# Optimization experiments

Measured on AMD Instinct MI355X. Metric: run time of the kernel, lower is better.

The kernel has to match this reference:

```python
import jax, jax.numpy as jnp
import numpy as np

N_FFT = 254
WIN = 254
HOP = 64
ITERS = 50
AUDIO_DIM = 16384
MAX_VALUE = 69.37411499023438


def _hann(n):
    # tf.signal.hann_window (periodic)
    return (0.5 - 0.5 * jnp.cos(2.0 * jnp.pi * jnp.arange(n) / n)).astype(jnp.float32)


def _synth_window():
    # tf.signal.inverse_stft_window_fn(HOP) applied to hann forward window
    w = _hann(WIN)
    overlaps = -(-WIN // HOP)
    d = jnp.pad(w * w, (0, overlaps * HOP - WIN))
    d = d.reshape(overlaps, HOP).sum(axis=0)  # overlap-added squared window per phase
    d = jnp.tile(d, overlaps)[:WIN]
    return w / d


def _stft(x, window):
    # x: [B, L] -> [B, F, N_FFT//2+1]; win_length == n_fft so no zero-padding of frames
    L = x.shape[1]
    nf = 1 + (L - WIN) // HOP
    idx = jnp.arange(nf)[:, None] * HOP + jnp.arange(WIN)
    frames = x[:, idx] * window
    return jnp.fft.rfft(frames, n=N_FFT)


def _istft(spec, swin, out_len):
    # spec: [B, F, bins] -> [B, out_len] via windowed overlap-add
    frames = jnp.fft.irfft(spec, n=N_FFT)[..., :WIN] * swin
    nf = frames.shape[1]
    idx = jnp.arange(nf)[:, None] * HOP + jnp.arange(WIN)
    out = jnp.zeros((frames.shape[0], out_len), frames.dtype)
    return out.at[:, idx].add(frames)


def setup_inputs() -> dict:
    key = jax.random.key(0)
    x = jax.random.uniform(key, (128, 256, 128, 1), dtype=jnp.float32)
    return {"x": x}


def reference(x):
    win = _hann(WIN)
    swin = _synth_window()
    # de-log / de-normalize the spectrogram
    mag = jnp.exp(5.0 * (x - 1.0)) * MAX_VALUE
    mag = jnp.squeeze(mag, -1)  # [B, F, 128]
    nframes = mag.shape[1]
    out_len = HOP * (nframes - 1) + WIN  # 16574

    # Griffin-Lim: initial reconstruction with zero phase
    waveform = _istft(mag.astype(jnp.complex64), swin, out_len)

    def step(wf, _):
        phase = jnp.angle(_stft(wf, win))
        spec = mag * jnp.exp(1j * phase)
        return _istft(spec, swin, out_len), None

    waveform, _ = jax.lax.scan(step, waveform, None, length=ITERS)

    waveform = waveform / jnp.max(jnp.abs(waveform))
    return waveform[:, :AUDIO_DIM, None]  # [B, 16384, 1]
```

## Files before the change

### kernel.cpp

```cpp
#include <hip/hip_runtime.h>
#include <math.h>


#define B_SZ 128
#define NFRM 256
#define BINS 128
#define NFFT 254
#define OUTL 16574
#define AUD  16384
#define GL_ITERS 50
#define MAXV 69.37411499023438f
#define PI2f 6.2831853071795864f

typedef __attribute__((ext_vector_type(8))) short short8;
typedef __attribute__((ext_vector_type(4))) short short4v;
typedef __attribute__((ext_vector_type(4))) float f32x4;

__device__ __forceinline__ unsigned short f2bf(float f) {
  unsigned u = __float_as_uint(f);
  return (unsigned short)((u + 0x7FFFu + ((u >> 16) & 1u)) >> 16);
}
__device__ __forceinline__ float bf2f(unsigned short h) {
  return __uint_as_float(((unsigned)h) << 16);
}
__device__ __forceinline__ void split3(float v, short* h, short* m, short* l) {
  unsigned short hh = f2bf(v);
  float r1 = v - bf2f(hh);
  unsigned short mm = f2bf(r1);
  float r2 = r1 - bf2f(mm);
  *h = (short)hh; *m = (short)mm; *l = (short)f2bf(r2);
}

__device__ __forceinline__ int slotf(int c, int row) {
  return (c & ~7) | ((c ^ row ^ (row >> 3)) & 7);
}

#define MFMA6(ACC, AH, AM, AL, BH, BM, BL)                                   \
  ACC = __builtin_amdgcn_mfma_f32_16x16x32_bf16(AH, BL, ACC, 0, 0, 0);       \
  ACC = __builtin_amdgcn_mfma_f32_16x16x32_bf16(AM, BM, ACC, 0, 0, 0);       \
  ACC = __builtin_amdgcn_mfma_f32_16x16x32_bf16(AL, BH, ACC, 0, 0, 0);       \
  ACC = __builtin_amdgcn_mfma_f32_16x16x32_bf16(AH, BM, ACC, 0, 0, 0);       \
  ACC = __builtin_amdgcn_mfma_f32_16x16x32_bf16(AM, BH, ACC, 0, 0, 0);       \
  ACC = __builtin_amdgcn_mfma_f32_16x16x32_bf16(AH, BH, ACC, 0, 0, 0);

__global__ void tables_k(short* __restrict__ WfH, short* __restrict__ WfM,
                         short* __restrict__ WfL, short* __restrict__ WiH,
                         short* __restrict__ WiM, short* __restrict__ WiL,
                         unsigned* __restrict__ gmax) {
  int tid = blockIdx.x * blockDim.x + threadIdx.x;
  if (tid == 0) *gmax = 0u;
  if (tid >= 65536) return;
  int idx = tid;
  int j = idx & 7, l = (idx >> 3) & 63, nt = (idx >> 9) & 15, kc = idx >> 13;
  int krow = kc * 32 + ((l >> 4) << 3) + j;
  int ncol = (nt << 4) + (l & 15);
  float v1 = 0.f;
  if (krow < NFFT) {
    int kk = ncol >> 1;
    int m = (kk * krow) % NFFT;
    float ang = PI2f * (float)m / (float)NFFT;
    float wn = 0.5f - 0.5f * cosf(PI2f * (float)krow / (float)NFFT);
    v1 = wn * ((ncol & 1) ? -sinf(ang) : cosf(ang));
  }
  split3(v1, &WfH[idx], &WfM[idx], &WfL[idx]);
  float v2 = 0.f;
  if (ncol < NFFT) {
    int kk = krow >> 1;
    int m = (kk * ncol) % NFFT;
    float ang = PI2f * (float)m / (float)NFFT;
    float wn = 0.5f - 0.5f * cosf(PI2f * (float)ncol / (float)NFFT);
    float d = 0.f;
    int p = ncol & 63;
    for (int q = 0; q < 4; ++q) {
      int nn = p + 64 * q;
      if (nn < NFFT) { float w = 0.5f - 0.5f * cosf(PI2f * (float)nn / (float)NFFT); d += w * w; }
    }
    float sw = wn / d;
    float ak = (kk == 0 || kk == BINS - 1) ? 1.f : 2.f;
    v2 = sw * (ak / (float)NFFT) * ((krow & 1) ? -sinf(ang) : cosf(ang));
  }
  split3(v2, &WiH[idx], &WiM[idx], &WiL[idx]);
}

__global__ void mag_k(const float* __restrict__ x, float* __restrict__ mag) {
  int i = blockIdx.x * 256 + threadIdx.x;
  mag[i] = expf(5.f * (x[i] - 1.f)) * MAXV;
}

template <int FIRST>
__global__ __launch_bounds__(512) void iter_k(
    const float* __restrict__ FRsrc, float* __restrict__ FRdst,
    const float* __restrict__ mag,
    const short* __restrict__ WfH, const short* __restrict__ WfM,
    const short* __restrict__ WfL,
    const short* __restrict__ WiH, const short* __restrict__ WiM,
    const short* __restrict__ WiL) {
  __shared__ __align__(16) short SH[8192], SM[8192], SL[8192];
  __shared__ __align__(16) char scratch[16640];
  short* wfsH = (short*)scratch;
  short* wfsM = wfsH + 2240;
  short* wfsL = wfsM + 2240;
  float* tr = (float*)scratch;

  int blk = blockIdx.x;
  int b = blk >> 3, f0 = (blk & 7) << 5;
  int tid = threadIdx.x, lane = tid & 63, wv = tid >> 6;
  int fgl = b * NFRM + f0;

  if (FIRST) {
    int row = tid >> 4;
#pragma unroll
    for (int q = 0; q < 2; ++q) {
      int c = ((tid & 15) << 1) + q;
      float4 mg = *(const float4*)&mag[((size_t)(fgl + row) << 7) + (c << 2)];
      short h[8] __attribute__((aligned(16))), m[8] __attribute__((aligned(16))),
            l[8] __attribute__((aligned(16)));
#pragma unroll
      for (int u = 0; u < 4; ++u) {
        split3(((const float*)&mg)[u], &h[2 * u], &m[2 * u], &l[2 * u]);
        h[2 * u + 1] = 0; m[2 * u + 1] = 0; l[2 * u + 1] = 0;
      }
      int p = (row << 8) + (slotf(c, row) << 3);
      *(short8*)&SH[p] = *(const short8*)h;
      *(short8*)&SM[p] = *(const short8*)m;
      *(short8*)&SL[p] = *(const short8*)l;
    }
  } else {
    const float* FRb = FRsrc + ((size_t)b << 16);
    for (int i4 = tid; i4 < 560; i4 += 512) {
      int i = i4 << 2;
      int t = (f0 << 6) + i;
      int ft = t >> 6, cb = t & 63;
      float4 s = make_float4(0.f, 0.f, 0.f, 0.f);
#pragma unroll
      for (int d = 3; d >= 0; --d) {
        int f = ft - d;
        if (f >= 0 && f <= 255) {
          float4 v = *(const float4*)&FRb[(f << 8) + cb + (d << 6)];
          s.x += v.x; s.y += v.y; s.z += v.z; s.w += v.w;
        }
      }
      if (i == 2236) { s.z = 0.f; s.w = 0.f; }
      short hh[4] __attribute__((aligned(8))), mm[4] __attribute__((aligned(8))),
            ll[4] __attribute__((aligned(8)));
      split3(s.x, &hh[0], &mm[0], &ll[0]);
      split3(s.y, &hh[1], &mm[1], &ll[1]);
      split3(s.z, &hh[2], &mm[2], &ll[2]);
      split3(s.w, &hh[3], &mm[3], &ll[3]);
      int q = i >> 3;
      int qs = (q & ~7) | ((q ^ (q >> 3)) & 7);
      int p = (qs << 3) | (i & 7);
      *(short4v*)&wfsH[p] = *(const short4v*)hh;
      *(short4v*)&wfsM[p] = *(const short4v*)mm;
      *(short4v*)&wfsL[p] = *(const short4v*)ll;
    }

    f32x4 acc1[2][2];
#pragma unroll
    for (int i = 0; i < 2; ++i) { acc1[i][0] = (f32x4){0,0,0,0}; acc1[i][1] = (f32x4){0,0,0,0}; }

    __syncthreads();

    for (int kc = 0; kc < 8; ++kc) {
      short8 Ah[2], Am[2], Al[2];
#pragma unroll
      for (int mt = 0; mt < 2; ++mt) {
        int frame = (mt << 4) + (lane & 15);
        int q = (frame << 3) + (kc << 2) + (lane >> 4);
        int qs = (q & ~7) | ((q ^ (q >> 3)) & 7);
        Ah[mt] = *(const short8*)&wfsH[qs << 3];
        Am[mt] = *(const short8*)&wfsM[qs << 3];
        Al[mt] = *(const short8*)&wfsL[qs << 3];
      }
#pragma unroll
      for (int nt = 0; nt < 2; ++nt) {
        int ntg = (wv << 1) + nt;
        size_t off = (((size_t)((kc << 4) + ntg) << 6) + lane) << 3;
        short8 bh = *(const short8*)(WfH + off);
        short8 bm = *(const short8*)(WfM + off);
        short8 bl = *(const short8*)(WfL + off);
#pragma unroll
        for (int mt = 0; mt < 2; ++mt) {
          MFMA6(acc1[mt][nt], Ah[mt], Am[mt], Al[mt], bh, bm, bl)
        }
      }
    }

    for (int mtg = 0; mtg < 2; ++mtg) {
      __syncthreads();
#pragma unroll
      for (int nt = 0; nt < 2; ++nt) {
        int col = (((wv << 1) + nt) << 4) | (lane & 15);
#pragma unroll
        for (int r = 0; r < 4; ++r) {
          int row16 = ((lane >> 4) << 2) + r;
          tr[row16 * 260 + col] = acc1[mtg][nt][r];
        }
      }
      __syncthreads();
      {
        int trow = tid >> 5;
        int c = tid & 31;
        int c0 = c << 3;
        float4 va = *(const float4*)&tr[trow * 260 + c0];
        float4 vb = *(const float4*)&tr[trow * 260 + c0 + 4];
        int lrow = (mtg << 4) + trow;
        int srow = fgl + lrow;
        float4 xm = *(const float4*)&mag[((size_t)srow << 7) + (c << 2)];
        float vv[8] = {va.x, va.y, va.z, va.w, vb.x, vb.y, vb.z, vb.w};
        short hh[8] __attribute__((aligned(16))), mm[8] __attribute__((aligned(16))),
              ll[8] __attribute__((aligned(16)));
#pragma unroll
        for (int pq = 0; pq < 4; ++pq) {
          float mg = ((const float*)&xm)[pq];
          float re = vv[2 * pq], im = vv[2 * pq + 1];
          float s2 = re * re + im * im;
          float oe, oo;
          if (s2 == 0.f) { oe = mg; oo = 0.f; }
          else { float rr = mg * rsqrtf(s2); oe = re * rr; oo = im * rr; }
          split3(oe, &hh[2 * pq], &mm[2 * pq], &ll[2 * pq]);
          split3(oo, &hh[2 * pq + 1], &mm[2 * pq + 1], &ll[2 * pq + 1]);
        }
        int p = (lrow << 8) + (slotf(c, lrow) << 3);
        *(short8*)&SH[p] = *(const short8*)hh;
        *(short8*)&SM[p] = *(const short8*)mm;
        *(short8*)&SL[p] = *(const short8*)ll;
      }
    }
  }

  f32x4 acc2[2][2];
#pragma unroll
  for (int i = 0; i < 2; ++i) { acc2[i][0] = (f32x4){0,0,0,0}; acc2[i][1] = (f32x4){0,0,0,0}; }

  __syncthreads();

  for (int kc = 0; kc < 8; ++kc) {
    short8 bh[2], bm[2], bl[2];
#pragma unroll
    for (int nt = 0; nt < 2; ++nt) {
      int ntg = (wv << 1) + nt;
      size_t off = (((size_t)((kc << 4) + ntg) << 6) + lane) << 3;
      bh[nt] = *(const short8*)(WiH + off);
      bm[nt] = *(const short8*)(WiM + off);
      bl[nt] = *(const short8*)(WiL + off);
    }
#pragma unroll
    for (int mt = 0; mt < 2; ++mt) {
      int rl = (mt << 4) + (lane & 15);
      int c = (kc << 2) + (lane >> 4);
      int base = (rl << 8) + (slotf(c, rl) << 3);
      short8 Ah = *(const short8*)&SH[base];
      short8 Am = *(const short8*)&SM[base];
      short8 Al = *(const short8*)&SL[base];
#pragma unroll
      for (int nt = 0; nt < 2; ++nt) {
        MFMA6(acc2[mt][nt], Ah, Am, Al, bh[nt], bm[nt], bl[nt])
      }
    }
  }

  float* FRo = FRdst + ((size_t)b << 16) + ((size_t)f0 << 8);
#pragma unroll
  for (int mt = 0; mt < 2; ++mt)
#pragma unroll
    for (int nt = 0; nt < 2; ++nt) {
      int col = (((wv << 1) + nt) << 4) | (lane & 15);
#pragma unroll
      for (int r = 0; r < 4; ++r) {
        int row = (mt << 4) + ((lane >> 4) << 2) + r;
        FRo[((size_t)row << 8) + col] = acc2[mt][nt][r];
      }
    }
}

__global__ void redmax_k(const float* __restrict__ FR, unsigned* __restrict__ gmax) {
  __shared__ float red[16];
  int b = blockIdx.x;
  const float* FRb = FR + ((size_t)b << 16);
  float v = 0.f;
  for (int t = threadIdx.x; t < OUTL; t += 1024) {
    int f_hi = t >> 6; if (f_hi > NFRM - 1) f_hi = NFRM - 1;
    int f_lo = (t >= NFFT) ? (((t - NFFT) >> 6) + 1) : 0;
    float s = 0.f;
    for (int f = f_lo; f <= f_hi; ++f) s += FRb[(f << 8) + t - (f << 6)];
    v = fmaxf(v, fabsf(s));
  }
#pragma unroll
  for (int o = 32; o > 0; o >>= 1) v = fmaxf(v, __shfl_xor(v, o, 64));
  if ((threadIdx.x & 63) == 0) red[threadIdx.x >> 6] = v;
  __syncthreads();
  if (threadIdx.x < 16) {
    v = red[threadIdx.x];
#pragma unroll
    for (int o = 8; o > 0; o >>= 1) v = fmaxf(v, __shfl_xor(v, o, 16));
    if (threadIdx.x == 0) atomicMax(gmax, __float_as_uint(v));
  }
}

__global__ void out_k(const float* __restrict__ FR, const unsigned* __restrict__ gmax,
                      float* __restrict__ out) {
  int b = blockIdx.y, t = blockIdx.x * 256 + threadIdx.x;
  const float* FRb = FR + ((size_t)b << 16);
  int f_hi = t >> 6; if (f_hi > NFRM - 1) f_hi = NFRM - 1;
  int f_lo = (t >= NFFT) ? (((t - NFFT) >> 6) + 1) : 0;
  float s = 0.f;
  for (int f = f_lo; f <= f_hi; ++f) s += FRb[(f << 8) + t - (f << 6)];
  float g = __uint_as_float(*gmax);
  out[(size_t)b * AUD + t] = s / g;
}

extern "C" void kernel_launch(void* const* d_in, const int* in_sizes, int n_in,
                              void* d_out, int out_size, void* d_ws, size_t ws_size,
                              hipStream_t stream) {
  const float* x = (const float*)d_in[0];

  float* FR0 = (float*)d_ws;
  float* FR1 = FR0 + 8388608;
  float* mag = FR1 + 8388608;
  short* WfH = (short*)(mag + 4194304);
  short* WfM = WfH + 65536;
  short* WfL = WfM + 65536;
  short* WiH = WfL + 65536;
  short* WiM = WiH + 65536;
  short* WiL = WiM + 65536;
  unsigned* gmax = (unsigned*)(WiL + 65536);

  mag_k<<<16384, 256, 0, stream>>>(x, mag);
  tables_k<<<256, 256, 0, stream>>>(WfH, WfM, WfL, WiH, WiM, WiL, gmax);

  iter_k<1><<<1024, 512, 0, stream>>>(FR1, FR0, mag, WfH, WfM, WfL, WiH, WiM, WiL);

  float* bufs[2] = {FR0, FR1};
  for (int it = 0; it < GL_ITERS; ++it) {
    iter_k<0><<<1024, 512, 0, stream>>>(bufs[it & 1], bufs[(it + 1) & 1], mag,
                                        WfH, WfM, WfL, WiH, WiM, WiL);
  }

  redmax_k<<<B_SZ, 1024, 0, stream>>>(FR0, gmax);
  out_k<<<dim3(64, B_SZ), 256, 0, stream>>>(FR0, gmax, (float*)d_out);
}
```

Measured before the change: 2.499 ms.

## Double-buffer DFT basis loads in registers and split transpose scratch

Prefetches the next k-chunk of the forward and inverse DFT basis fragments into registers while the current chunk's MFMAs run, and preloads the first inverse chunk before the phase-projection stage. This is meant to hide global-memory latency for basis loads. It also splits the transpose scratch into two half-buffers with stride 132 to cut LDS bank conflicts. The extra live short8 registers raise register pressure, which could lower occupancy.

```diff
diff --git a/kernel.cpp b/kernel.cpp
--- a/kernel.cpp
+++ b/kernel.cpp
@@ -96,16 +96,20 @@
     const short* __restrict__ WiH, const short* __restrict__ WiM,
     const short* __restrict__ WiL) {
   __shared__ __align__(16) short SH[8192], SM[8192], SL[8192];
-  __shared__ __align__(16) char scratch[16640];
+  __shared__ __align__(16) char scratch[16896];
   short* wfsH = (short*)scratch;
   short* wfsM = wfsH + 2240;
   short* wfsL = wfsM + 2240;
-  float* tr = (float*)scratch;
+  float* trA = (float*)scratch;
+  float* trB = trA + 2112;
 
   int blk = blockIdx.x;
   int b = blk >> 3, f0 = (blk & 7) << 5;
   int tid = threadIdx.x, lane = tid & 63, wv = tid >> 6;
   int fgl = b * NFRM + f0;
+  int ntg0 = (wv << 1), ntg1 = ntg0 + 1;
+
+  short8 g2h[2][2], g2m[2][2], g2l[2][2];
 
   if (FIRST) {
     int row = tid >> 4;
@@ -125,7 +129,23 @@
       *(short8*)&SM[p] = *(const short8*)m;
       *(short8*)&SL[p] = *(const short8*)l;
     }
+    {
+      size_t o0 = (((size_t)ntg0 << 6) + lane) << 3;
+      size_t o1 = (((size_t)ntg1 << 6) + lane) << 3;
+      g2h[0][0] = *(const short8*)(WiH + o0); g2h[0][1] = *(const short8*)(WiH + o1);
+      g2m[0][0] = *(const short8*)(WiM + o0); g2m[0][1] = *(const short8*)(WiM + o1);
+      g2l[0][0] = *(const short8*)(WiL + o0); g2l[0][1] = *(const short8*)(WiL + o1);
+    }
   } else {
+    short8 g1h[2][2], g1m[2][2], g1l[2][2];
+    {
+      size_t o0 = (((size_t)ntg0 << 6) + lane) << 3;
+      size_t o1 = (((size_t)ntg1 << 6) + lane) << 3;
+      g1h[0][0] = *(const short8*)(WfH + o0); g1h[0][1] = *(const short8*)(WfH + o1);
+      g1m[0][0] = *(const short8*)(WfM + o0); g1m[0][1] = *(const short8*)(WfM + o1);
+      g1l[0][0] = *(const short8*)(WfL + o0); g1l[0][1] = *(const short8*)(WfL + o1);
+    }
+
     const float* FRb = FRsrc + ((size_t)b << 16);
     for (int i4 = tid; i4 < 560; i4 += 512) {
       int i = i4 << 2;
@@ -161,7 +181,16 @@
 
     __syncthreads();
 
+#pragma unroll
     for (int kc = 0; kc < 8; ++kc) {
+      const int cur = kc & 1, nxt = cur ^ 1;
+      if (kc < 7) {
+        size_t o0 = (((size_t)(((kc + 1) << 4) + ntg0) << 6) + lane) << 3;
+        size_t o1 = (((size_t)(((kc + 1) << 4) + ntg1) << 6) + lane) << 3;
+        g1h[nxt][0] = *(const short8*)(WfH + o0); g1h[nxt][1] = *(const short8*)(WfH + o1);
+        g1m[nxt][0] = *(const short8*)(WfM + o0); g1m[nxt][1] = *(const short8*)(WfM + o1);
+        g1l[nxt][0] = *(const short8*)(WfL + o0); g1l[nxt][1] = *(const short8*)(WfL + o1);
+      }
       short8 Ah[2], Am[2], Al[2];
 #pragma unroll
       for (int mt = 0; mt < 2; ++mt) {
@@ -173,17 +202,19 @@
         Al[mt] = *(const short8*)&wfsL[qs << 3];
       }
 #pragma unroll
-      for (int nt = 0; nt < 2; ++nt) {
-        int ntg = (wv << 1) + nt;
-        size_t off = (((size_t)((kc << 4) + ntg) << 6) + lane) << 3;
-        short8 bh = *(const short8*)(WfH + off);
-        short8 bm = *(const short8*)(WfM + off);
-        short8 bl = *(const short8*)(WfL + off);
+      for (int nt = 0; nt < 2; ++nt)
 #pragma unroll
         for (int mt = 0; mt < 2; ++mt) {
-          MFMA6(acc1[mt][nt], Ah[mt], Am[mt], Al[mt], bh, bm, bl)
+          MFMA6(acc1[mt][nt], Ah[mt], Am[mt], Al[mt], g1h[cur][nt], g1m[cur][nt], g1l[cur][nt])
         }
-      }
+    }
+
+    {
+      size_t o0 = (((size_t)ntg0 << 6) + lane) << 3;
+      size_t o1 = (((size_t)ntg1 << 6) + lane) << 3;
+      g2h[0][0] = *(const short8*)(WiH + o0); g2h[0][1] = *(const short8*)(WiH + o1);
+      g2m[0][0] = *(const short8*)(WiM + o0); g2m[0][1] = *(const short8*)(WiM + o1);
+      g2l[0][0] = *(const short8*)(WiL + o0); g2l[0][1] = *(const short8*)(WiL + o1);
     }
 
     for (int mtg = 0; mtg < 2; ++mtg) {
@@ -191,19 +222,21 @@
 #pragma unroll
       for (int nt = 0; nt < 2; ++nt) {
         int col = (((wv << 1) + nt) << 4) | (lane & 15);
+        int cc = col >> 3, hb = (col >> 2) & 1, w = col & 3;
+        float* th = hb ? trB : trA;
+        int base = (cc << 2) + w;
 #pragma unroll
         for (int r = 0; r < 4; ++r) {
           int row16 = ((lane >> 4) << 2) + r;
-          tr[row16 * 260 + col] = acc1[mtg][nt][r];
+          th[row16 * 132 + base] = acc1[mtg][nt][r];
         }
       }
       __syncthreads();
       {
         int trow = tid >> 5;
         int c = tid & 31;
-        int c0 = c << 3;
-        float4 va = *(const float4*)&tr[trow * 260 + c0];
-        float4 vb = *(const float4*)&tr[trow * 260 + c0 + 4];
+        float4 va = *(const float4*)&trA[trow * 132 + (c << 2)];
+        float4 vb = *(const float4*)&trB[trow * 132 + (c << 2)];
         int lrow = (mtg << 4) + trow;
         int srow = fgl + lrow;
         float4 xm = *(const float4*)&mag[((size_t)srow << 7) + (c << 2)];
@@ -235,15 +268,15 @@
 
   __syncthreads();
 
+#pragma unroll
   for (int kc = 0; kc < 8; ++kc) {
-    short8 bh[2], bm[2], bl[2];
-#pragma unroll
-    for (int nt = 0; nt < 2; ++nt) {
-      int ntg = (wv << 1) + nt;
-      size_t off = (((size_t)((kc << 4) + ntg) << 6) + lane) << 3;
-      bh[nt] = *(const short8*)(WiH + off);
-      bm[nt] = *(const short8*)(WiM + off);
-      bl[nt] = *(const short8*)(WiL + off);
+    const int cur = kc & 1, nxt = cur ^ 1;
+    if (kc < 7) {
+      size_t o0 = (((size_t)(((kc + 1) << 4) + ntg0) << 6) + lane) << 3;
+      size_t o1 = (((size_t)(((kc + 1) << 4) + ntg1) << 6) + lane) << 3;
+      g2h[nxt][0] = *(const short8*)(WiH + o0); g2h[nxt][1] = *(const short8*)(WiH + o1);
+      g2m[nxt][0] = *(const short8*)(WiM + o0); g2m[nxt][1] = *(const short8*)(WiM + o1);
+      g2l[nxt][0] = *(const short8*)(WiL + o0); g2l[nxt][1] = *(const short8*)(WiL + o1);
     }
 #pragma unroll
     for (int mt = 0; mt < 2; ++mt) {
@@ -255,7 +288,7 @@
       short8 Al = *(const short8*)&SL[base];
 #pragma unroll
       for (int nt = 0; nt < 2; ++nt) {
-        MFMA6(acc2[mt][nt], Ah, Am, Al, bh[nt], bm[nt], bl[nt])
+        MFMA6(acc2[mt][nt], Ah, Am, Al, g2h[cur][nt], g2m[cur][nt], g2l[cur][nt])
       }
     }
   }
```

Result: no change. 2.524 ms (+1.0%).

## Exploit real-signal symmetry in inverse DFT to halve iSTFT matmul work

Applied to the files above, without the earlier changes.

The inverse real DFT is split into a cosine part on the real spectrum and a sine part on the imaginary spectrum. Each part covers only the first half of the output samples, and the mirrored samples come from the sum and difference C±S. The synthesis window is applied in the epilogue instead of being folded into the table. This halves the MFMA count and the inverse-table loads of the second GEMM, at the cost of a new spectrum layout in LDS, an extra window table, and edge-case handling at n=0, n=127 and indices 254/255.

```diff
diff --git a/kernel.cpp b/kernel.cpp
--- a/kernel.cpp
+++ b/kernel.cpp
@@ -30,7 +30,6 @@
   float r2 = r1 - bf2f(mm);
   *h = (short)hh; *m = (short)mm; *l = (short)f2bf(r2);
 }
-
 __device__ __forceinline__ int slotf(int c, int row) {
   return (c & ~7) | ((c ^ row ^ (row >> 3)) & 7);
 }
@@ -44,42 +43,49 @@
   ACC = __builtin_amdgcn_mfma_f32_16x16x32_bf16(AH, BH, ACC, 0, 0, 0);
 
 __global__ void tables_k(short* __restrict__ WfH, short* __restrict__ WfM,
-                         short* __restrict__ WfL, short* __restrict__ WiH,
-                         short* __restrict__ WiM, short* __restrict__ WiL,
+                         short* __restrict__ WfL, short* __restrict__ CI,
+                         short* __restrict__ SI, float* __restrict__ swin,
                          unsigned* __restrict__ gmax) {
   int tid = blockIdx.x * blockDim.x + threadIdx.x;
   if (tid == 0) *gmax = 0u;
-  if (tid >= 65536) return;
-  int idx = tid;
-  int j = idx & 7, l = (idx >> 3) & 63, nt = (idx >> 9) & 15, kc = idx >> 13;
-  int krow = kc * 32 + ((l >> 4) << 3) + j;
-  int ncol = (nt << 4) + (l & 15);
-  float v1 = 0.f;
-  if (krow < NFFT) {
-    int kk = ncol >> 1;
-    int m = (kk * krow) % NFFT;
+  if (tid < 256) {
+    float v = 0.f;
+    if (tid < NFFT) {
+      float wn = 0.5f - 0.5f * cosf(PI2f * (float)tid / (float)NFFT);
+      float d = 0.f;
+      int p = tid & 63;
+      for (int q = 0; q < 4; ++q) {
+        int nn = p + 64 * q;
+        if (nn < NFFT) { float w = 0.5f - 0.5f * cosf(PI2f * (float)nn / (float)NFFT); d += w * w; }
+      }
+      v = wn / d;
+    }
+    swin[tid] = v;
+  }
+  if (tid < 65536) {
+    int j = tid & 7, l = (tid >> 3) & 63, nt = (tid >> 9) & 15, kc = tid >> 13;
+    int krow = kc * 32 + ((l >> 4) << 3) + j;
+    int ncol = (nt << 4) + (l & 15);
+    float v1 = 0.f;
+    if (krow < NFFT) {
+      int kk = ncol >> 1;
+      int m = (kk * krow) % NFFT;
+      float ang = PI2f * (float)m / (float)NFFT;
+      float wn = 0.5f - 0.5f * cosf(PI2f * (float)krow / (float)NFFT);
+      v1 = wn * ((ncol & 1) ? -sinf(ang) : cosf(ang));
+    }
+    split3(v1, &WfH[tid], &WfM[tid], &WfL[tid]);
+  }
+  if (tid < 16384) {
+    int j = tid & 7, l = (tid >> 3) & 63;
+    int krow = (tid >> 12) * 32 + ((l >> 4) << 3) + j;
+    int ncol = (((tid >> 9) & 7) << 4) + (l & 15);
+    int m = (krow * ncol) % NFFT;
     float ang = PI2f * (float)m / (float)NFFT;
-    float wn = 0.5f - 0.5f * cosf(PI2f * (float)krow / (float)NFFT);
-    v1 = wn * ((ncol & 1) ? -sinf(ang) : cosf(ang));
-  }
-  split3(v1, &WfH[idx], &WfM[idx], &WfL[idx]);
-  float v2 = 0.f;
-  if (ncol < NFFT) {
-    int kk = krow >> 1;
-    int m = (kk * ncol) % NFFT;
-    float ang = PI2f * (float)m / (float)NFFT;
-    float wn = 0.5f - 0.5f * cosf(PI2f * (float)ncol / (float)NFFT);
-    float d = 0.f;
-    int p = ncol & 63;
-    for (int q = 0; q < 4; ++q) {
-      int nn = p + 64 * q;
-      if (nn < NFFT) { float w = 0.5f - 0.5f * cosf(PI2f * (float)nn / (float)NFFT); d += w * w; }
-    }
-    float sw = wn / d;
-    float ak = (kk == 0 || kk == BINS - 1) ? 1.f : 2.f;
-    v2 = sw * (ak / (float)NFFT) * ((krow & 1) ? -sinf(ang) : cosf(ang));
-  }
-  split3(v2, &WiH[idx], &WiM[idx], &WiL[idx]);
+    float sc = ((krow == 0 || krow == BINS - 1) ? 1.f : 2.f) / (float)NFFT;
+    split3(sc * cosf(ang), &CI[tid], &CI[16384 + tid], &CI[32768 + tid]);
+    split3(-sc * sinf(ang), &SI[tid], &SI[16384 + tid], &SI[32768 + tid]);
+  }
 }
 
 __global__ void mag_k(const float* __restrict__ x, float* __restrict__ mag) {
@@ -90,17 +96,17 @@
 template <int FIRST>
 __global__ __launch_bounds__(512) void iter_k(
     const float* __restrict__ FRsrc, float* __restrict__ FRdst,
-    const float* __restrict__ mag,
+    const float* __restrict__ mag, const float* __restrict__ swin,
     const short* __restrict__ WfH, const short* __restrict__ WfM,
     const short* __restrict__ WfL,
-    const short* __restrict__ WiH, const short* __restrict__ WiM,
-    const short* __restrict__ WiL) {
-  __shared__ __align__(16) short SH[8192], SM[8192], SL[8192];
-  __shared__ __align__(16) char scratch[16640];
+    const short* __restrict__ CI, const short* __restrict__ SI) {
+  __shared__ __align__(16) short Y[24576];
+  __shared__ __align__(16) char scratch[16896];
   short* wfsH = (short*)scratch;
   short* wfsM = wfsH + 2240;
   short* wfsL = wfsM + 2240;
-  float* tr = (float*)scratch;
+  float* trA = (float*)scratch;
+  float* trB = trA + 2112;
 
   int blk = blockIdx.x;
   int b = blk >> 3, f0 = (blk & 7) << 5;
@@ -108,23 +114,22 @@
   int fgl = b * NFRM + f0;
 
   if (FIRST) {
-    int row = tid >> 4;
-#pragma unroll
-    for (int q = 0; q < 2; ++q) {
-      int c = ((tid & 15) << 1) + q;
-      float4 mg = *(const float4*)&mag[((size_t)(fgl + row) << 7) + (c << 2)];
-      short h[8] __attribute__((aligned(16))), m[8] __attribute__((aligned(16))),
-            l[8] __attribute__((aligned(16)));
-#pragma unroll
-      for (int u = 0; u < 4; ++u) {
-        split3(((const float*)&mg)[u], &h[2 * u], &m[2 * u], &l[2 * u]);
-        h[2 * u + 1] = 0; m[2 * u + 1] = 0; l[2 * u + 1] = 0;
-      }
-      int p = (row << 8) + (slotf(c, row) << 3);
-      *(short8*)&SH[p] = *(const short8*)h;
-      *(short8*)&SM[p] = *(const short8*)m;
-      *(short8*)&SL[p] = *(const short8*)l;
-    }
+    int row = tid >> 4, q = tid & 15;
+    int srow = fgl + row;
+    float4 m0 = *(const float4*)&mag[((size_t)srow << 7) + (q << 3)];
+    float4 m1 = *(const float4*)&mag[((size_t)srow << 7) + (q << 3) + 4];
+    float mv[8] = {m0.x, m0.y, m0.z, m0.w, m1.x, m1.y, m1.z, m1.w};
+    short h[8] __attribute__((aligned(16))), m[8] __attribute__((aligned(16))),
+          l[8] __attribute__((aligned(16))), z[8] __attribute__((aligned(16)));
+#pragma unroll
+    for (int e = 0; e < 8; ++e) { split3(mv[e], &h[e], &m[e], &l[e]); z[e] = 0; }
+    int off = (row << 7) + (slotf(q, row) << 3);
+    *(short8*)&Y[off]         = *(const short8*)h;
+    *(short8*)&Y[4096 + off]  = *(const short8*)m;
+    *(short8*)&Y[8192 + off]  = *(const short8*)l;
+    *(short8*)&Y[12288 + off] = *(const short8*)z;
+    *(short8*)&Y[16384 + off] = *(const short8*)z;
+    *(short8*)&Y[20480 + off] = *(const short8*)z;
   } else {
     const float* FRb = FRsrc + ((size_t)b << 16);
     for (int i4 = tid; i4 < 560; i4 += 512) {
@@ -191,87 +196,101 @@
 #pragma unroll
       for (int nt = 0; nt < 2; ++nt) {
         int col = (((wv << 1) + nt) << 4) | (lane & 15);
+        int cc = col >> 3, hb = (col >> 2) & 1, w = col & 3;
+        float* th = hb ? trB : trA;
+        int base = (cc << 2) + w;
 #pragma unroll
         for (int r = 0; r < 4; ++r) {
           int row16 = ((lane >> 4) << 2) + r;
-          tr[row16 * 260 + col] = acc1[mtg][nt][r];
+          th[row16 * 132 + base] = acc1[mtg][nt][r];
         }
       }
       __syncthreads();
       {
         int trow = tid >> 5;
         int c = tid & 31;
-        int c0 = c << 3;
-        float4 va = *(const float4*)&tr[trow * 260 + c0];
-        float4 vb = *(const float4*)&tr[trow * 260 + c0 + 4];
+        float4 va = *(const float4*)&trA[trow * 132 + (c << 2)];
+        float4 vb = *(const float4*)&trB[trow * 132 + (c << 2)];
         int lrow = (mtg << 4) + trow;
         int srow = fgl + lrow;
         float4 xm = *(const float4*)&mag[((size_t)srow << 7) + (c << 2)];
         float vv[8] = {va.x, va.y, va.z, va.w, vb.x, vb.y, vb.z, vb.w};
-        short hh[8] __attribute__((aligned(16))), mm[8] __attribute__((aligned(16))),
-              ll[8] __attribute__((aligned(16)));
+        short reh[4] __attribute__((aligned(8))), rem[4] __attribute__((aligned(8))),
+              rel[4] __attribute__((aligned(8))), imh[4] __attribute__((aligned(8))),
+              imm[4] __attribute__((aligned(8))), iml[4] __attribute__((aligned(8)));
 #pragma unroll
         for (int pq = 0; pq < 4; ++pq) {
           float mg = ((const float*)&xm)[pq];
           float re = vv[2 * pq], im = vv[2 * pq + 1];
           float s2 = re * re + im * im;
-          float oe, oo;
-          if (s2 == 0.f) { oe = mg; oo = 0.f; }
-          else { float rr = mg * rsqrtf(s2); oe = re * rr; oo = im * rr; }
-          split3(oe, &hh[2 * pq], &mm[2 * pq], &ll[2 * pq]);
-          split3(oo, &hh[2 * pq + 1], &mm[2 * pq + 1], &ll[2 * pq + 1]);
+          float ore, oim;
+          if (s2 == 0.f) { ore = mg; oim = 0.f; }
+          else { float rr = mg * rsqrtf(s2); ore = re * rr; oim = im * rr; }
+          split3(ore, &reh[pq], &rem[pq], &rel[pq]);
+          split3(oim, &imh[pq], &imm[pq], &iml[pq]);
         }
-        int p = (lrow << 8) + (slotf(c, lrow) << 3);
-        *(short8*)&SH[p] = *(const short8*)hh;
-        *(short8*)&SM[p] = *(const short8*)mm;
-        *(short8*)&SL[p] = *(const short8*)ll;
-      }
-    }
-  }
-
-  f32x4 acc2[2][2];
-#pragma unroll
-  for (int i = 0; i < 2; ++i) { acc2[i][0] = (f32x4){0,0,0,0}; acc2[i][1] = (f32x4){0,0,0,0}; }
+        int c2 = c >> 1, half = (c & 1) << 2;
+        int off2 = (lrow << 7) + (slotf(c2, lrow) << 3) + half;
+        *(short4v*)&Y[off2]         = *(const short4v*)reh;
+        *(short4v*)&Y[4096 + off2]  = *(const short4v*)rem;
+        *(short4v*)&Y[8192 + off2]  = *(const short4v*)rel;
+        *(short4v*)&Y[12288 + off2] = *(const short4v*)imh;
+        *(short4v*)&Y[16384 + off2] = *(const short4v*)imm;
+        *(short4v*)&Y[20480 + off2] = *(const short4v*)iml;
+      }
+    }
+  }
+
+  f32x4 aC[2], aS[2];
+#pragma unroll
+  for (int i = 0; i < 2; ++i) { aC[i] = (f32x4){0,0,0,0}; aS[i] = (f32x4){0,0,0,0}; }
 
   __syncthreads();
 
-  for (int kc = 0; kc < 8; ++kc) {
-    short8 bh[2], bm[2], bl[2];
-#pragma unroll
-    for (int nt = 0; nt < 2; ++nt) {
-      int ntg = (wv << 1) + nt;
-      size_t off = (((size_t)((kc << 4) + ntg) << 6) + lane) << 3;
-      bh[nt] = *(const short8*)(WiH + off);
-      bm[nt] = *(const short8*)(WiM + off);
-      bl[nt] = *(const short8*)(WiL + off);
-    }
+  for (int kc = 0; kc < 4; ++kc) {
+    short8 ReH[2], ReM[2], ReL[2], ImH[2], ImM[2], ImL[2];
 #pragma unroll
     for (int mt = 0; mt < 2; ++mt) {
       int rl = (mt << 4) + (lane & 15);
       int c = (kc << 2) + (lane >> 4);
-      int base = (rl << 8) + (slotf(c, rl) << 3);
-      short8 Ah = *(const short8*)&SH[base];
-      short8 Am = *(const short8*)&SM[base];
-      short8 Al = *(const short8*)&SL[base];
-#pragma unroll
-      for (int nt = 0; nt < 2; ++nt) {
-        MFMA6(acc2[mt][nt], Ah, Am, Al, bh[nt], bm[nt], bl[nt])
-      }
-    }
-  }
-
-  float* FRo = FRdst + ((size_t)b << 16) + ((size_t)f0 << 8);
-#pragma unroll
-  for (int mt = 0; mt < 2; ++mt)
-#pragma unroll
-    for (int nt = 0; nt < 2; ++nt) {
-      int col = (((wv << 1) + nt) << 4) | (lane & 15);
+      int off = (rl << 7) + (slotf(c, rl) << 3);
+      ReH[mt] = *(const short8*)&Y[off];
+      ReM[mt] = *(const short8*)&Y[4096 + off];
+      ReL[mt] = *(const short8*)&Y[8192 + off];
+      ImH[mt] = *(const short8*)&Y[12288 + off];
+      ImM[mt] = *(const short8*)&Y[16384 + off];
+      ImL[mt] = *(const short8*)&Y[20480 + off];
+    }
+    size_t flat = (((size_t)((kc << 3) + wv) << 6) + lane) << 3;
+    short8 ch = *(const short8*)(CI + flat);
+    short8 cm = *(const short8*)(CI + 16384 + flat);
+    short8 cl = *(const short8*)(CI + 32768 + flat);
+    short8 sh = *(const short8*)(SI + flat);
+    short8 sm = *(const short8*)(SI + 16384 + flat);
+    short8 sl = *(const short8*)(SI + 32768 + flat);
+#pragma unroll
+    for (int mt = 0; mt < 2; ++mt) {
+      MFMA6(aC[mt], ReH[mt], ReM[mt], ReL[mt], ch, cm, cl)
+      MFMA6(aS[mt], ImH[mt], ImM[mt], ImL[mt], sh, sm, sl)
+    }
+  }
+
+  {
+    int n = (wv << 4) + (lane & 15);
+    float swn = swin[n];
+    float swp = swin[254 - n];
+    float* FRo = FRdst + ((size_t)b << 16) + ((size_t)f0 << 8);
+#pragma unroll
+    for (int mt = 0; mt < 2; ++mt)
 #pragma unroll
       for (int r = 0; r < 4; ++r) {
         int row = (mt << 4) + ((lane >> 4) << 2) + r;
-        FRo[((size_t)row << 8) + col] = acc2[mt][nt][r];
-      }
-    }
+        float C = aC[mt][r], S_ = aS[mt][r];
+        FRo[((size_t)row << 8) + n] = swn * (C + S_);
+        if (n >= 1 && n <= 126) FRo[((size_t)row << 8) + 254 - n] = swp * (C - S_);
+        if (n == 0) { FRo[((size_t)row << 8) + 254] = 0.f; FRo[((size_t)row << 8) + 255] = 0.f; }
+      }
+  }
 }
 
 __global__ void redmax_k(const float* __restrict__ FR, unsigned* __restrict__ gmax) {
@@ -321,20 +340,20 @@
   short* WfH = (short*)(mag + 4194304);
   short* WfM = WfH + 65536;
   short* WfL = WfM + 65536;
-  short* WiH = WfL + 65536;
-  short* WiM = WiH + 65536;
-  short* WiL = WiM + 65536;
-  unsigned* gmax = (unsigned*)(WiL + 65536);
+  short* CI  = WfL + 65536;
+  short* SI  = CI + 49152;
+  float* swin = (float*)(SI + 49152);
+  unsigned* gmax = (unsigned*)(swin + 256);
 
   mag_k<<<16384, 256, 0, stream>>>(x, mag);
-  tables_k<<<256, 256, 0, stream>>>(WfH, WfM, WfL, WiH, WiM, WiL, gmax);
-
-  iter_k<1><<<1024, 512, 0, stream>>>(FR1, FR0, mag, WfH, WfM, WfL, WiH, WiM, WiL);
+  tables_k<<<256, 256, 0, stream>>>(WfH, WfM, WfL, CI, SI, swin, gmax);
+
+  iter_k<1><<<1024, 512, 0, stream>>>(FR1, FR0, mag, swin, WfH, WfM, WfL, CI, SI);
 
   float* bufs[2] = {FR0, FR1};
   for (int it = 0; it < GL_ITERS; ++it) {
-    iter_k<0><<<1024, 512, 0, stream>>>(bufs[it & 1], bufs[(it + 1) & 1], mag,
-                                        WfH, WfM, WfL, WiH, WiM, WiL);
+    iter_k<0><<<1024, 512, 0, stream>>>(bufs[it & 1], bufs[(it + 1) & 1], mag, swin,
+                                        WfH, WfM, WfL, CI, SI);
   }
 
   redmax_k<<<B_SZ, 1024, 0, stream>>>(FR0, gmax);
```

After: 2.190 ms. 12.4% less time.
